# Optimization experiments

Hardware: AMD Instinct MI355X
Metric: run time of the kernel (lower is better)

The kernel has to match this reference:

```python
import jax, jax.numpy as jnp
import numpy as np

B, S, HID = 2, 2048, 2048
H, HKV = 16, 4
D = HID // H          # 128
N_REP = H // HKV      # 4
ROPE_THETA = 1000000.0


def _rope_tables(seq_len, head_dim, theta):
    inv_freq = 1.0 / (theta ** (jnp.arange(0, head_dim, 2, dtype=jnp.float32) / head_dim))
    freqs = jnp.arange(seq_len, dtype=jnp.float32)[:, None] * inv_freq[None, :]  # [S, D/2]
    emb = jnp.concatenate([freqs, freqs], axis=-1)  # [S, D]
    return jnp.cos(emb), jnp.sin(emb)


def setup_inputs() -> dict:
    key = jax.random.key(0)
    ks = jax.random.split(key, 6)
    cos, sin = _rope_tables(S, D, ROPE_THETA)
    sc = 0.02
    return {
        "x": jax.random.normal(ks[0], (B, S, HID), jnp.float32),
        "cos": cos,
        "sin": sin,
        "Wq": jax.random.normal(ks[1], (HID, H * D), jnp.float32) * sc,
        "Wk": jax.random.normal(ks[2], (HID, HKV * D), jnp.float32) * sc,
        "Wv": jax.random.normal(ks[3], (HID, HKV * D), jnp.float32) * sc,
        "Wo": jax.random.normal(ks[4], (H * D, HID), jnp.float32) * sc,
    }


def _rotate_half(t):
    t1, t2 = jnp.split(t, 2, axis=-1)
    return jnp.concatenate([-t2, t1], axis=-1)


def reference(x, cos, sin, Wq, Wk, Wv, Wo):
    b, s, _ = x.shape
    q = (x @ Wq).reshape(b, s, H, D)    # [b,s,H,d]
    k = (x @ Wk).reshape(b, s, HKV, D)  # [b,s,Hkv,d]
    v = (x @ Wv).reshape(b, s, HKV, D)

    # RoPE (cos/sin broadcast over head axis)
    c = cos[:s, None, :]  # [s,1,d]
    sn = sin[:s, None, :]
    q = q * c + _rotate_half(q) * sn
    k = k * c + _rotate_half(k) * sn

    # GQA: repeat kv heads (interleaved, matching repeat_kv)
    k = jnp.repeat(k, N_REP, axis=2)  # [b,s,H,d]
    v = jnp.repeat(v, N_REP, axis=2)

    q = q.transpose(0, 2, 1, 3)  # [b,H,s,d]
    k = k.transpose(0, 2, 1, 3)
    v = v.transpose(0, 2, 1, 3)

    scale = 1.0 / jnp.sqrt(jnp.asarray(D, x.dtype))
    scores = jnp.einsum("bhqd,bhkd->bhqk", q, k) * scale
    causal = jnp.tril(jnp.ones((s, s), dtype=bool))
    scores = jnp.where(causal[None, None], scores, jnp.asarray(-jnp.inf, scores.dtype))
    probs = jax.nn.softmax(scores, axis=-1)
    out = jnp.einsum("bhqk,bhkd->bhqd", probs, v)
    out = out.transpose(0, 2, 1, 3).reshape(b, s, H * D)
    return out @ Wo
```

## Files before the change

### kernel.cpp

```cpp
#include <hip/hip_runtime.h>
#include <cstdint>

#define B_    2
#define S_    2048
#define HID_  2048
#define H_    16
#define HKV_  4
#define D_    128
#define SCALE_ 0.08838834764831845f
#define LOG2E_ 1.4426950408889634f
#define K1_   (SCALE_ * LOG2E_)
#define THRS_ 62.75f

typedef __bf16 bf16x8 __attribute__((ext_vector_type(8)));
typedef float  f32x4  __attribute__((ext_vector_type(4)));
using u16 = unsigned short;

static __device__ __forceinline__ u16 f2bf(float f) {
  union { float f; uint32_t u; } c; c.f = f;
  uint32_t u = c.u;
  return (u16)((u + 0x7FFFu + ((u >> 16) & 1u)) >> 16);
}
static __device__ __forceinline__ float bf2f(u16 h) {
  union { uint32_t u; float f; } c; c.u = ((uint32_t)h) << 16;
  return c.f;
}
static __device__ __forceinline__ void async16(const u16* g, u16* lds) {
  __builtin_amdgcn_global_load_lds((const __attribute__((address_space(1))) void*)g,
                                   (__attribute__((address_space(3))) void*)lds, 16, 0, 0);
}

__global__ __launch_bounds__(256) void prep_cast_weights(const float* __restrict__ x,
                                                         const float* __restrict__ Wq,
                                                         const float* __restrict__ Wk,
                                                         const float* __restrict__ Wv,
                                                         const float* __restrict__ Wo,
                                                         u16* __restrict__ xb,
                                                         u16* __restrict__ Wt,
                                                         u16* __restrict__ Wot) {
  __shared__ float tile[32][33];
  const int t = blockIdx.x;
  const int tid = threadIdx.x;
  if (t < 8192) {
    const int i = t * 256 + tid;
    float4 v = ((const float4*)x)[i];
    ushort4 o;
    o.x = f2bf(v.x); o.y = f2bf(v.y); o.z = f2bf(v.z); o.w = f2bf(v.w);
    ((ushort4*)xb)[i] = o;
    return;
  }
  const int tw = t - 8192;
  const float* W; u16* Dst; int N, lt;
  if (tw < 4096)      { W = Wq; Dst = Wt;                        N = 2048; lt = tw; }
  else if (tw < 5120) { W = Wk; Dst = Wt + (size_t)2048 * 2048;  N = 512;  lt = tw - 4096; }
  else if (tw < 6144) { W = Wv; Dst = Wt + (size_t)2560 * 2048;  N = 512;  lt = tw - 5120; }
  else                { W = Wo; Dst = Wot;                       N = 2048; lt = tw - 6144; }
  const int tx = tid & 31, ty = tid >> 5;
  const int tn = N >> 5;
  const int n0 = (lt % tn) * 32, k0 = (lt / tn) * 32;
#pragma unroll
  for (int j = 0; j < 32; j += 8)
    tile[ty + j][tx] = W[(size_t)(k0 + ty + j) * N + n0 + tx];
  __syncthreads();
#pragma unroll
  for (int j = 0; j < 32; j += 8)
    Dst[(size_t)(n0 + ty + j) * 2048 + k0 + tx] = f2bf(tile[tx][ty + j]);
}

__global__ __launch_bounds__(256) void prep_rope_vt(const u16* __restrict__ qkv,
                                                    const float* __restrict__ cosb,
                                                    const float* __restrict__ sinb,
                                                    u16* __restrict__ Qr, u16* __restrict__ Kr,
                                                    u16* __restrict__ Vt) {
  __shared__ u16 tile[32][34];
  const int NQ = B_ * S_ * H_ * 64;
  const int NK = B_ * S_ * HKV_ * 64;
  const int blk = blockIdx.x;
  const int tid = threadIdx.x;
  if (blk < 20480) {
    const int idx = blk * 256 + tid;
    if (idx < NQ) {
      const int j = idx & 63, rest = idx >> 6;
      const int h = rest & 15, srow = rest >> 4;
      const int s = srow & (S_ - 1);
      const u16* base = qkv + (size_t)srow * 3072 + h * 128;
      const float c = cosb[s * 128 + j], sn = sinb[s * 128 + j];
      const float a = bf2f(base[j]), b2 = bf2f(base[j + 64]);
      const size_t qo = (((size_t)(srow >> 11) * H_ + h) * S_ + s) * D_;
      Qr[qo + j]      = f2bf(a * c - b2 * sn);
      Qr[qo + j + 64] = f2bf(b2 * c + a * sn);
    } else if (idx < NQ + NK) {
      const int t2 = idx - NQ;
      const int j = t2 & 63, rest = t2 >> 6;
      const int kv = rest & 3, srow = rest >> 2;
      const int s = srow & (S_ - 1);
      const u16* base = qkv + (size_t)srow * 3072 + 2048 + kv * 128;
      const float c = cosb[s * 128 + j], sn = sinb[s * 128 + j];
      const float a = bf2f(base[j]), b2 = bf2f(base[j + 64]);
      const size_t ko = (((size_t)(srow >> 11) * HKV_ + kv) * S_ + s) * D_;
      Kr[ko + j]      = f2bf(a * c - b2 * sn);
      Kr[ko + j + 64] = f2bf(b2 * c + a * sn);
    }
    return;
  }
  const int lt = blk - 20480;
  const int bx = lt & 3, by = (lt >> 2) & 63, mat = lt >> 8;
  const int b = mat >> 2, kv = mat & 3;
  const int d0 = bx * 32, s0 = by * 32;
  const int tx = tid & 31, ty = tid >> 5;
#pragma unroll
  for (int j = 0; j < 32; j += 8)
    tile[ty + j][tx] = qkv[(size_t)(b * S_ + s0 + ty + j) * 3072 + 2560 + kv * 128 + d0 + tx];
  __syncthreads();
  const int sc  = s0 + tx;
  const int t64 = sc & 63;
  const int p   = ((t64 >> 5) * 4 + ((t64 >> 2) & 3)) * 8 + ((t64 >> 4) & 1) * 4 + (t64 & 3);
  const int scp = (sc & ~63) | p;
#pragma unroll
  for (int j = 0; j < 32; j += 8)
    Vt[((size_t)mat * D_ + d0 + ty + j) * S_ + scp] = tile[tx][ty + j];
}

template<int BF16OUT>
__global__ __launch_bounds__(256, 4) void gemm_bt(const u16* __restrict__ A,
                                                  const u16* __restrict__ Bt,
                                                  void* __restrict__ Cv,
                                                  int M, int N, int K, int gx) {
  const int nwg = (int)gridDim.x;
  const int bid = (int)blockIdx.x;
  const int qq = nwg >> 3, rr = nwg & 7;
  const int xcd = bid & 7, pos = bid >> 3;
  const int wg = ((xcd < rr) ? xcd * (qq + 1) : rr * (qq + 1) + (xcd - rr) * qq) + pos;
  const int bm = (wg % gx) * 128;
  const int bn = (wg / gx) * 128;

  __shared__ __align__(16) u16 Ash[128 * 64];
  __shared__ __align__(16) u16 Bsh[128 * 64];
  const int tid = threadIdx.x;
  const int w = tid >> 6, l = tid & 63;
  const int wm = (w >> 1) * 64, wn = (w & 1) * 64;

  const f32x4 z4 = {0.f, 0.f, 0.f, 0.f};
  f32x4 acc[4][4];
#pragma unroll
  for (int i = 0; i < 4; ++i)
#pragma unroll
    for (int j = 0; j < 4; ++j) acc[i][j] = z4;

  const int srow = w * 8 + (l >> 3);
  const int schunk = l & 7;

  for (int k0 = 0; k0 < K; k0 += 64) {
#pragma unroll
    for (int i = 0; i < 4; ++i) {
      const int row = i * 32 + srow;
      const int ch = schunk ^ (row & 7);
      async16(A + (size_t)(bm + row) * K + k0 + ch * 8, &Ash[(i * 4 + w) * 512]);
      async16(Bt + (size_t)(bn + row) * K + k0 + ch * 8, &Bsh[(i * 4 + w) * 512]);
    }
    asm volatile("s_waitcnt vmcnt(0)" ::: "memory");
    __syncthreads();
#pragma unroll
    for (int kc = 0; kc < 2; ++kc) {
      bf16x8 af[4], bfr[4];
#pragma unroll
      for (int mi = 0; mi < 4; ++mi) {
        const int r = wm + mi * 16 + (l & 15);
        const int c2 = (kc * 4 + (l >> 4)) ^ (r & 7);
        af[mi] = *(const bf16x8*)&Ash[r * 64 + c2 * 8];
      }
#pragma unroll
      for (int ni = 0; ni < 4; ++ni) {
        const int r = wn + ni * 16 + (l & 15);
        const int c2 = (kc * 4 + (l >> 4)) ^ (r & 7);
        bfr[ni] = *(const bf16x8*)&Bsh[r * 64 + c2 * 8];
      }
#pragma unroll
      for (int mi = 0; mi < 4; ++mi)
#pragma unroll
        for (int ni = 0; ni < 4; ++ni)
          acc[mi][ni] = __builtin_amdgcn_mfma_f32_16x16x32_bf16(af[mi], bfr[ni], acc[mi][ni], 0, 0, 0);
    }
    __syncthreads();
  }
#pragma unroll
  for (int mi = 0; mi < 4; ++mi) {
    const int r0 = bm + wm + mi * 16 + ((l >> 4) << 2);
#pragma unroll
    for (int ni = 0; ni < 4; ++ni) {
      const int c = bn + wn + ni * 16 + (l & 15);
#pragma unroll
      for (int j = 0; j < 4; ++j) {
        if (BF16OUT) ((u16*)Cv)[(size_t)(r0 + j) * N + c] = f2bf(acc[mi][ni][j]);
        else         ((float*)Cv)[(size_t)(r0 + j) * N + c] = acc[mi][ni][j];
      }
    }
  }
}

__global__ __launch_bounds__(256, 3) void attn_kernel(const u16* __restrict__ Q,
                                                      const u16* __restrict__ Kc,
                                                      const u16* __restrict__ Vt,
                                                      u16* __restrict__ O) {
  const int bid = blockIdx.x;
  const int bh  = bid & 31;
  const int pr  = bid >> 5;
  const int b   = bh >> 4;
  const int kvh = (bh & 15) >> 2;
  const int tid = threadIdx.x;
  const int w = tid >> 6, l = tid & 63;
  const int g = l >> 4, c = l & 15;

  __shared__ __align__(16) u16 Ksh[64 * 128];
  __shared__ __align__(16) u16 VshF[2 * 128 * 64];

  const u16* Kbase = Kc + ((size_t)(b * HKV_ + kvh) * S_) * D_;
  const u16* Vbase = Vt + ((size_t)(b * HKV_ + kvh) * D_) * S_;

  int srcK[4], srcV[4];
#pragma unroll
  for (int i = 0; i < 4; ++i) {
    const int rK = i * 16 + w * 4 + g;
    srcK[i] = rK * 128 + (c ^ (rK & 7)) * 8;
    const int dV = i * 32 + w * 8 + (l >> 3);
    srcV[i] = dV * S_ + ((l & 7) ^ (dV & 7)) * 8;
  }

  auto stageK = [&](int kv0) {
#pragma unroll
    for (int i = 0; i < 4; ++i)
      async16(Kbase + (size_t)kv0 * 128 + srcK[i], &Ksh[i * 2048 + w * 512]);
  };
  auto stageV = [&](int buf, int kv0) {
#pragma unroll
    for (int i = 0; i < 4; ++i)
      async16(Vbase + kv0 + srcV[i], &VshF[buf * 8192 + i * 2048 + w * 512]);
  };

  const f32x4 z4 = {0.f, 0.f, 0.f, 0.f};

#pragma unroll 1
  for (int seg = 0; seg < 2; ++seg) {
    const int qt = seg ? pr : (31 - pr);
    const int q0 = qt * 64;
    const int nt = qt + 1;

    bf16x8 qf[4];
    {
      const u16* qp = Q + ((size_t)bh * S_ + q0 + w * 16 + c) * D_ + g * 8;
#pragma unroll
      for (int kc = 0; kc < 4; ++kc) qf[kc] = *(const bf16x8*)(qp + kc * 32);
    }

    f32x4 oacc[8];
#pragma unroll
    for (int nb = 0; nb < 8; ++nb) oacc[nb] = z4;
    float m_i = -1e30f, l_i = 0.f;

    if (seg) __syncthreads();
    stageV(0, 0);
    stageK(0);

    for (int t = 0; t < nt; ++t) {
      const int cur = t & 1;
      asm volatile("s_waitcnt vmcnt(0)" ::: "memory");
      __syncthreads();
      if (t + 1 < nt) stageV(cur ^ 1, (t + 1) << 6);

      f32x4 sf[4];
#pragma unroll
      for (int nb = 0; nb < 4; ++nb) sf[nb] = z4;

      __builtin_amdgcn_s_setprio(1);
#pragma unroll
      for (int kc = 0; kc < 4; ++kc) {
#pragma unroll
        for (int nb = 0; nb < 4; ++nb) {
          const int r = nb * 16 + c;
          const int s2 = (kc * 4 + g) ^ (c & 7);
          const bf16x8 kf = *(const bf16x8*)&Ksh[r * 128 + s2 * 8];
          sf[nb] = __builtin_amdgcn_mfma_f32_16x16x32_bf16(kf, qf[kc], sf[nb], 0, 0, 0);
        }
      }
      __builtin_amdgcn_s_setprio(0);

      __syncthreads();
      if (t + 1 < nt) stageK((t + 1) << 6);

      {
        const int kv0 = t << 6;
        const int qcol = q0 + w * 16 + c;
        const bool doMask = (t == nt - 1);
        float mx = -3e38f;
#pragma unroll
        for (int nb = 0; nb < 4; ++nb)
#pragma unroll
          for (int jj = 0; jj < 4; ++jj) {
            float sv = sf[nb][jj];
            if (doMask) {
              const int kk = kv0 + nb * 16 + g * 4 + jj;
              sv = (kk > qcol) ? -3e38f : sv;
              sf[nb][jj] = sv;
            }
            mx = fmaxf(mx, sv);
          }
        mx = fmaxf(mx, __shfl_xor(mx, 16));
        mx = fmaxf(mx, __shfl_xor(mx, 32));

        if (__all(mx <= m_i + THRS_)) {
          const float mk = m_i * K1_;
          float rs = 0.f;
#pragma unroll
          for (int nb = 0; nb < 4; ++nb)
#pragma unroll
            for (int jj = 0; jj < 4; ++jj) {
              const float p = exp2f(fmaf(sf[nb][jj], K1_, -mk));
              sf[nb][jj] = p;
              rs += p;
            }
          rs += __shfl_xor(rs, 16);
          rs += __shfl_xor(rs, 32);
          l_i += rs;
        } else {
          const float mnew = fmaxf(m_i, mx);
          const float fsc = exp2f((m_i - mnew) * K1_);
          m_i = mnew;
          const float mk = mnew * K1_;
          float rs = 0.f;
#pragma unroll
          for (int nb = 0; nb < 4; ++nb)
#pragma unroll
            for (int jj = 0; jj < 4; ++jj) {
              const float p = exp2f(fmaf(sf[nb][jj], K1_, -mk));
              sf[nb][jj] = p;
              rs += p;
            }
          rs += __shfl_xor(rs, 16);
          rs += __shfl_xor(rs, 32);
          l_i = l_i * fsc + rs;
          float fq[4];
#pragma unroll
          for (int j = 0; j < 4; ++j) fq[j] = __shfl(fsc, g * 4 + j);
#pragma unroll
          for (int nb = 0; nb < 8; ++nb)
#pragma unroll
            for (int j = 0; j < 4; ++j) oacc[nb][j] *= fq[j];
        }
      }

      bf16x8 pa, pb;
#pragma unroll
      for (int jj = 0; jj < 4; ++jj) {
        pa[jj] = (__bf16)sf[0][jj]; pa[4 + jj] = (__bf16)sf[1][jj];
        pb[jj] = (__bf16)sf[2][jj]; pb[4 + jj] = (__bf16)sf[3][jj];
      }

      const char* Vb = (const char*)&VshF[cur * 8192] + c * 128;
      __builtin_amdgcn_s_setprio(1);
#pragma unroll
      for (int kc2 = 0; kc2 < 2; ++kc2) {
        const bf16x8 pfr = kc2 ? pb : pa;
        const int s2v = ((kc2 * 4 + g) ^ (c & 7)) << 4;
#pragma unroll
        for (int nb = 0; nb < 8; ++nb) {
          const bf16x8 vf = *(const bf16x8*)(Vb + nb * 2048 + s2v);
          oacc[nb] = __builtin_amdgcn_mfma_f32_16x16x32_bf16(pfr, vf, oacc[nb], 0, 0, 0);
        }
      }
      __builtin_amdgcn_s_setprio(0);
    }

#pragma unroll
    for (int j = 0; j < 4; ++j) {
      const float li = __shfl(l_i, g * 4 + j);
      const float inv = 1.f / li;
      const int srow = q0 + w * 16 + g * 4 + j;
      u16* op = O + ((size_t)(b * S_ + srow)) * HID_ + (bh & 15) * D_ + c;
#pragma unroll
      for (int nb = 0; nb < 8; ++nb) op[nb * 16] = f2bf(oacc[nb][j] * inv);
    }
  }
}

extern "C" void kernel_launch(void* const* d_in, const int* in_sizes, int n_in,
                              void* d_out, int out_size, void* d_ws, size_t ws_size,
                              hipStream_t stream) {
  const float* x    = (const float*)d_in[0];
  const float* cosb = (const float*)d_in[1];
  const float* sinb = (const float*)d_in[2];
  const float* Wq   = (const float*)d_in[3];
  const float* Wk   = (const float*)d_in[4];
  const float* Wv   = (const float*)d_in[5];
  const float* Wo   = (const float*)d_in[6];
  float* out = (float*)d_out;

  u16*   xb   = (u16*)d_ws;
  u16*   Wt   = xb  + (size_t)4096 * 2048;
  u16*   Wot  = Wt  + (size_t)3072 * 2048;
  u16*   qkv  = Wot + (size_t)2048 * 2048;
  u16*   Qr   = qkv + (size_t)4096 * 3072;
  u16*   Kr   = Qr  + (size_t)B_ * H_ * S_ * D_;
  u16*   Vtb  = Kr  + (size_t)B_ * HKV_ * S_ * D_;
  u16*   Ob   = Vtb + (size_t)B_ * HKV_ * S_ * D_;

  prep_cast_weights<<<dim3(18432), 256, 0, stream>>>(x, Wq, Wk, Wv, Wo, xb, Wt, Wot);

  gemm_bt<1><<<dim3(768), 256, 0, stream>>>(xb, Wt, qkv, 4096, 3072, 2048, 32);

  prep_rope_vt<<<dim3(22528), 256, 0, stream>>>(qkv, cosb, sinb, Qr, Kr, Vtb);

  attn_kernel<<<dim3(512), 256, 0, stream>>>(Qr, Kr, Vtb, Ob);

  gemm_bt<0><<<dim3(512), 256, 0, stream>>>(Ob, Wot, out, 4096, 2048, 2048, 32);
}
```

Before: 208.6 us.

## Split attention into one q-tile per block with GQA-grouped ordering; vectorize RoPE

The attention kernel now launches 1024 blocks, each handling a single 64-row query tile. Before, 512 blocks each processed a balanced pair of tiles. Block IDs are ordered so that the four query heads sharing a KV head, across both batches, run adjacently, starting with the longest causal tiles, to improve L2 reuse of K/V and load balance. The RoPE prep kernel now processes two elements per thread with float2/ushort2 loads and stores, halving its block count. The trade-off is less intrinsic balancing per block, relying on the hardware scheduler and the longest-first order instead.

```diff
diff --git a/kernel.cpp b/kernel.cpp
--- a/kernel.cpp
+++ b/kernel.cpp
@@ -73,37 +73,51 @@
                                                     u16* __restrict__ Qr, u16* __restrict__ Kr,
                                                     u16* __restrict__ Vt) {
   __shared__ u16 tile[32][34];
-  const int NQ = B_ * S_ * H_ * 64;
-  const int NK = B_ * S_ * HKV_ * 64;
+  const int NQ2 = B_ * S_ * H_ * 32;
+  const int NK2 = B_ * S_ * HKV_ * 32;
   const int blk = blockIdx.x;
   const int tid = threadIdx.x;
-  if (blk < 20480) {
+  if (blk < 10240) {
     const int idx = blk * 256 + tid;
-    if (idx < NQ) {
-      const int j = idx & 63, rest = idx >> 6;
+    if (idx < NQ2) {
+      const int j = (idx & 31) * 2, rest = idx >> 5;
       const int h = rest & 15, srow = rest >> 4;
       const int s = srow & (S_ - 1);
       const u16* base = qkv + (size_t)srow * 3072 + h * 128;
-      const float c = cosb[s * 128 + j], sn = sinb[s * 128 + j];
-      const float a = bf2f(base[j]), b2 = bf2f(base[j + 64]);
+      const float2 cc = *(const float2*)&cosb[s * 128 + j];
+      const float2 ss = *(const float2*)&sinb[s * 128 + j];
+      const ushort2 av = *(const ushort2*)&base[j];
+      const ushort2 bv = *(const ushort2*)&base[j + 64];
+      const float a0 = bf2f(av.x), a1 = bf2f(av.y);
+      const float b0 = bf2f(bv.x), b1 = bf2f(bv.y);
       const size_t qo = (((size_t)(srow >> 11) * H_ + h) * S_ + s) * D_;
-      Qr[qo + j]      = f2bf(a * c - b2 * sn);
-      Qr[qo + j + 64] = f2bf(b2 * c + a * sn);
-    } else if (idx < NQ + NK) {
-      const int t2 = idx - NQ;
-      const int j = t2 & 63, rest = t2 >> 6;
+      ushort2 lo, hi;
+      lo.x = f2bf(a0 * cc.x - b0 * ss.x); lo.y = f2bf(a1 * cc.y - b1 * ss.y);
+      hi.x = f2bf(b0 * cc.x + a0 * ss.x); hi.y = f2bf(b1 * cc.y + a1 * ss.y);
+      *(ushort2*)&Qr[qo + j]      = lo;
+      *(ushort2*)&Qr[qo + j + 64] = hi;
+    } else if (idx < NQ2 + NK2) {
+      const int t2 = idx - NQ2;
+      const int j = (t2 & 31) * 2, rest = t2 >> 5;
       const int kv = rest & 3, srow = rest >> 2;
       const int s = srow & (S_ - 1);
       const u16* base = qkv + (size_t)srow * 3072 + 2048 + kv * 128;
-      const float c = cosb[s * 128 + j], sn = sinb[s * 128 + j];
-      const float a = bf2f(base[j]), b2 = bf2f(base[j + 64]);
+      const float2 cc = *(const float2*)&cosb[s * 128 + j];
+      const float2 ss = *(const float2*)&sinb[s * 128 + j];
+      const ushort2 av = *(const ushort2*)&base[j];
+      const ushort2 bv = *(const ushort2*)&base[j + 64];
+      const float a0 = bf2f(av.x), a1 = bf2f(av.y);
+      const float b0 = bf2f(bv.x), b1 = bf2f(bv.y);
       const size_t ko = (((size_t)(srow >> 11) * HKV_ + kv) * S_ + s) * D_;
-      Kr[ko + j]      = f2bf(a * c - b2 * sn);
-      Kr[ko + j + 64] = f2bf(b2 * c + a * sn);
+      ushort2 lo, hi;
+      lo.x = f2bf(a0 * cc.x - b0 * ss.x); lo.y = f2bf(a1 * cc.y - b1 * ss.y);
+      hi.x = f2bf(b0 * cc.x + a0 * ss.x); hi.y = f2bf(b1 * cc.y + a1 * ss.y);
+      *(ushort2*)&Kr[ko + j]      = lo;
+      *(ushort2*)&Kr[ko + j + 64] = hi;
     }
     return;
   }
-  const int lt = blk - 20480;
+  const int lt = blk - 10240;
   const int bx = lt & 3, by = (lt >> 2) & 63, mat = lt >> 8;
   const int b = mat >> 2, kv = mat & 3;
   const int d0 = bx * 32, s0 = by * 32;
@@ -203,19 +217,30 @@
                                                       const u16* __restrict__ Vt,
                                                       u16* __restrict__ O) {
   const int bid = blockIdx.x;
-  const int bh  = bid & 31;
-  const int pr  = bid >> 5;
-  const int b   = bh >> 4;
-  const int kvh = (bh & 15) >> 2;
+  const int p   = bid & 7;
+  const int hs  = (bid >> 3) & 3;
+  const int qt  = 31 - (bid >> 5);
+  const int b   = p >> 2;
+  const int kvh = p & 3;
+  const int h   = kvh * 4 + hs;
+  const int bh  = b * 16 + h;
   const int tid = threadIdx.x;
   const int w = tid >> 6, l = tid & 63;
   const int g = l >> 4, c = l & 15;
+  const int q0 = qt * 64;
 
   __shared__ __align__(16) u16 Ksh[64 * 128];
   __shared__ __align__(16) u16 VshF[2 * 128 * 64];
 
   const u16* Kbase = Kc + ((size_t)(b * HKV_ + kvh) * S_) * D_;
   const u16* Vbase = Vt + ((size_t)(b * HKV_ + kvh) * D_) * S_;
+
+  bf16x8 qf[4];
+  {
+    const u16* qp = Q + ((size_t)bh * S_ + q0 + w * 16 + c) * D_ + g * 8;
+#pragma unroll
+    for (int kc = 0; kc < 4; ++kc) qf[kc] = *(const bf16x8*)(qp + kc * 32);
+  }
 
   int srcK[4], srcV[4];
 #pragma unroll
@@ -226,6 +251,12 @@
     srcV[i] = dV * S_ + ((l & 7) ^ (dV & 7)) * 8;
   }
 
+  const f32x4 z4 = {0.f, 0.f, 0.f, 0.f};
+  f32x4 oacc[8];
+#pragma unroll
+  for (int nb = 0; nb < 8; ++nb) oacc[nb] = z4;
+  float m_i = -1e30f, l_i = 0.f;
+
   auto stageK = [&](int kv0) {
 #pragma unroll
     for (int i = 0; i < 4; ++i)
@@ -237,148 +268,127 @@
       async16(Vbase + kv0 + srcV[i], &VshF[buf * 8192 + i * 2048 + w * 512]);
   };
 
-  const f32x4 z4 = {0.f, 0.f, 0.f, 0.f};
-
-#pragma unroll 1
-  for (int seg = 0; seg < 2; ++seg) {
-    const int qt = seg ? pr : (31 - pr);
-    const int q0 = qt * 64;
-    const int nt = qt + 1;
-
-    bf16x8 qf[4];
+  const int nt = qt + 1;
+  stageV(0, 0);
+  stageK(0);
+
+  for (int t = 0; t < nt; ++t) {
+    const int cur = t & 1;
+    asm volatile("s_waitcnt vmcnt(0)" ::: "memory");
+    __syncthreads();
+    if (t + 1 < nt) stageV(cur ^ 1, (t + 1) << 6);
+
+    f32x4 sf[4];
+#pragma unroll
+    for (int nb = 0; nb < 4; ++nb) sf[nb] = z4;
+
+    __builtin_amdgcn_s_setprio(1);
+#pragma unroll
+    for (int kc = 0; kc < 4; ++kc) {
+#pragma unroll
+      for (int nb = 0; nb < 4; ++nb) {
+        const int r = nb * 16 + c;
+        const int s2 = (kc * 4 + g) ^ (c & 7);
+        const bf16x8 kf = *(const bf16x8*)&Ksh[r * 128 + s2 * 8];
+        sf[nb] = __builtin_amdgcn_mfma_f32_16x16x32_bf16(kf, qf[kc], sf[nb], 0, 0, 0);
+      }
+    }
+    __builtin_amdgcn_s_setprio(0);
+
+    __syncthreads();
+    if (t + 1 < nt) stageK((t + 1) << 6);
+
     {
-      const u16* qp = Q + ((size_t)bh * S_ + q0 + w * 16 + c) * D_ + g * 8;
-#pragma unroll
-      for (int kc = 0; kc < 4; ++kc) qf[kc] = *(const bf16x8*)(qp + kc * 32);
-    }
-
-    f32x4 oacc[8];
-#pragma unroll
-    for (int nb = 0; nb < 8; ++nb) oacc[nb] = z4;
-    float m_i = -1e30f, l_i = 0.f;
-
-    if (seg) __syncthreads();
-    stageV(0, 0);
-    stageK(0);
-
-    for (int t = 0; t < nt; ++t) {
-      const int cur = t & 1;
-      asm volatile("s_waitcnt vmcnt(0)" ::: "memory");
-      __syncthreads();
-      if (t + 1 < nt) stageV(cur ^ 1, (t + 1) << 6);
-
-      f32x4 sf[4];
-#pragma unroll
-      for (int nb = 0; nb < 4; ++nb) sf[nb] = z4;
-
-      __builtin_amdgcn_s_setprio(1);
-#pragma unroll
-      for (int kc = 0; kc < 4; ++kc) {
-#pragma unroll
-        for (int nb = 0; nb < 4; ++nb) {
-          const int r = nb * 16 + c;
-          const int s2 = (kc * 4 + g) ^ (c & 7);
-          const bf16x8 kf = *(const bf16x8*)&Ksh[r * 128 + s2 * 8];
-          sf[nb] = __builtin_amdgcn_mfma_f32_16x16x32_bf16(kf, qf[kc], sf[nb], 0, 0, 0);
+      const int kv0 = t << 6;
+      const int qcol = q0 + w * 16 + c;
+      const bool doMask = (t == nt - 1);
+      float mx = -3e38f;
+#pragma unroll
+      for (int nb = 0; nb < 4; ++nb)
+#pragma unroll
+        for (int jj = 0; jj < 4; ++jj) {
+          float sv = sf[nb][jj];
+          if (doMask) {
+            const int kk = kv0 + nb * 16 + g * 4 + jj;
+            sv = (kk > qcol) ? -3e38f : sv;
+            sf[nb][jj] = sv;
+          }
+          mx = fmaxf(mx, sv);
         }
-      }
-      __builtin_amdgcn_s_setprio(0);
-
-      __syncthreads();
-      if (t + 1 < nt) stageK((t + 1) << 6);
-
-      {
-        const int kv0 = t << 6;
-        const int qcol = q0 + w * 16 + c;
-        const bool doMask = (t == nt - 1);
-        float mx = -3e38f;
+      mx = fmaxf(mx, __shfl_xor(mx, 16));
+      mx = fmaxf(mx, __shfl_xor(mx, 32));
+
+      if (__all(mx <= m_i + THRS_)) {
+        const float mk = m_i * K1_;
+        float rs = 0.f;
 #pragma unroll
         for (int nb = 0; nb < 4; ++nb)
 #pragma unroll
           for (int jj = 0; jj < 4; ++jj) {
-            float sv = sf[nb][jj];
-            if (doMask) {
-              const int kk = kv0 + nb * 16 + g * 4 + jj;
-              sv = (kk > qcol) ? -3e38f : sv;
-              sf[nb][jj] = sv;
-            }
-            mx = fmaxf(mx, sv);
+            const float p2 = exp2f(fmaf(sf[nb][jj], K1_, -mk));
+            sf[nb][jj] = p2;
+            rs += p2;
           }
-        mx = fmaxf(mx, __shfl_xor(mx, 16));
-        mx = fmaxf(mx, __shfl_xor(mx, 32));
-
-        if (__all(mx <= m_i + THRS_)) {
-          const float mk = m_i * K1_;
-          float rs = 0.f;
-#pragma unroll
-          for (int nb = 0; nb < 4; ++nb)
-#pragma unroll
-            for (int jj = 0; jj < 4; ++jj) {
-              const float p = exp2f(fmaf(sf[nb][jj], K1_, -mk));
-              sf[nb][jj] = p;
-              rs += p;
-            }
-          rs += __shfl_xor(rs, 16);
-          rs += __shfl_xor(rs, 32);
-          l_i += rs;
-        } else {
-          const float mnew = fmaxf(m_i, mx);
-          const float fsc = exp2f((m_i - mnew) * K1_);
-          m_i = mnew;
-          const float mk = mnew * K1_;
-          float rs = 0.f;
-#pragma unroll
-          for (int nb = 0; nb < 4; ++nb)
-#pragma unroll
-            for (int jj = 0; jj < 4; ++jj) {
-              const float p = exp2f(fmaf(sf[nb][jj], K1_, -mk));
-              sf[nb][jj] = p;
-              rs += p;
-            }
-          rs += __shfl_xor(rs, 16);
-          rs += __shfl_xor(rs, 32);
-          l_i = l_i * fsc + rs;
-          float fq[4];
-#pragma unroll
-          for (int j = 0; j < 4; ++j) fq[j] = __shfl(fsc, g * 4 + j);
-#pragma unroll
-          for (int nb = 0; nb < 8; ++nb)
-#pragma unroll
-            for (int j = 0; j < 4; ++j) oacc[nb][j] *= fq[j];
-        }
-      }
-
-      bf16x8 pa, pb;
-#pragma unroll
-      for (int jj = 0; jj < 4; ++jj) {
-        pa[jj] = (__bf16)sf[0][jj]; pa[4 + jj] = (__bf16)sf[1][jj];
-        pb[jj] = (__bf16)sf[2][jj]; pb[4 + jj] = (__bf16)sf[3][jj];
-      }
-
-      const char* Vb = (const char*)&VshF[cur * 8192] + c * 128;
-      __builtin_amdgcn_s_setprio(1);
-#pragma unroll
-      for (int kc2 = 0; kc2 < 2; ++kc2) {
-        const bf16x8 pfr = kc2 ? pb : pa;
-        const int s2v = ((kc2 * 4 + g) ^ (c & 7)) << 4;
-#pragma unroll
-        for (int nb = 0; nb < 8; ++nb) {
-          const bf16x8 vf = *(const bf16x8*)(Vb + nb * 2048 + s2v);
-          oacc[nb] = __builtin_amdgcn_mfma_f32_16x16x32_bf16(pfr, vf, oacc[nb], 0, 0, 0);
-        }
-      }
-      __builtin_amdgcn_s_setprio(0);
-    }
-
-#pragma unroll
-    for (int j = 0; j < 4; ++j) {
-      const float li = __shfl(l_i, g * 4 + j);
-      const float inv = 1.f / li;
-      const int srow = q0 + w * 16 + g * 4 + j;
-      u16* op = O + ((size_t)(b * S_ + srow)) * HID_ + (bh & 15) * D_ + c;
-#pragma unroll
-      for (int nb = 0; nb < 8; ++nb) op[nb * 16] = f2bf(oacc[nb][j] * inv);
-    }
+        rs += __shfl_xor(rs, 16);
+        rs += __shfl_xor(rs, 32);
+        l_i += rs;
+      } else {
+        const float mnew = fmaxf(m_i, mx);
+        const float fsc = exp2f((m_i - mnew) * K1_);
+        m_i = mnew;
+        const float mk = mnew * K1_;
+        float rs = 0.f;
+#pragma unroll
+        for (int nb = 0; nb < 4; ++nb)
+#pragma unroll
+          for (int jj = 0; jj < 4; ++jj) {
+            const float p2 = exp2f(fmaf(sf[nb][jj], K1_, -mk));
+            sf[nb][jj] = p2;
+            rs += p2;
+          }
+        rs += __shfl_xor(rs, 16);
+        rs += __shfl_xor(rs, 32);
+        l_i = l_i * fsc + rs;
+        float fq[4];
+#pragma unroll
+        for (int j = 0; j < 4; ++j) fq[j] = __shfl(fsc, g * 4 + j);
+#pragma unroll
+        for (int nb = 0; nb < 8; ++nb)
+#pragma unroll
+          for (int j = 0; j < 4; ++j) oacc[nb][j] *= fq[j];
+      }
+    }
+
+    bf16x8 pa, pb;
+#pragma unroll
+    for (int jj = 0; jj < 4; ++jj) {
+      pa[jj] = (__bf16)sf[0][jj]; pa[4 + jj] = (__bf16)sf[1][jj];
+      pb[jj] = (__bf16)sf[2][jj]; pb[4 + jj] = (__bf16)sf[3][jj];
+    }
+
+    const char* Vb = (const char*)&VshF[cur * 8192] + c * 128;
+    __builtin_amdgcn_s_setprio(1);
+#pragma unroll
+    for (int kc2 = 0; kc2 < 2; ++kc2) {
+      const bf16x8 pfr = kc2 ? pb : pa;
+      const int s2v = ((kc2 * 4 + g) ^ (c & 7)) << 4;
+#pragma unroll
+      for (int nb = 0; nb < 8; ++nb) {
+        const bf16x8 vf = *(const bf16x8*)(Vb + nb * 2048 + s2v);
+        oacc[nb] = __builtin_amdgcn_mfma_f32_16x16x32_bf16(pfr, vf, oacc[nb], 0, 0, 0);
+      }
+    }
+    __builtin_amdgcn_s_setprio(0);
+  }
+
+#pragma unroll
+  for (int j = 0; j < 4; ++j) {
+    const float li = __shfl(l_i, g * 4 + j);
+    const float inv = 1.f / li;
+    const int srow = q0 + w * 16 + g * 4 + j;
+    u16* op = O + ((size_t)(b * S_ + srow)) * HID_ + h * D_ + c;
+#pragma unroll
+    for (int nb = 0; nb < 8; ++nb) op[nb * 16] = f2bf(oacc[nb][j] * inv);
   }
 }
 
@@ -407,9 +417,9 @@
 
   gemm_bt<1><<<dim3(768), 256, 0, stream>>>(xb, Wt, qkv, 4096, 3072, 2048, 32);
 
-  prep_rope_vt<<<dim3(22528), 256, 0, stream>>>(qkv, cosb, sinb, Qr, Kr, Vtb);
-
-  attn_kernel<<<dim3(512), 256, 0, stream>>>(Qr, Kr, Vtb, Ob);
+  prep_rope_vt<<<dim3(12288), 256, 0, stream>>>(qkv, cosb, sinb, Qr, Kr, Vtb);
+
+  attn_kernel<<<dim3(1024), 256, 0, stream>>>(Qr, Kr, Vtb, Ob);
 
   gemm_bt<0><<<dim3(512), 256, 0, stream>>>(Ob, Wot, out, 4096, 2048, 2048, 32);
 }
```

New measurement: 198.6 us. 4.8% less time.
